# Optimization experiments

Measured on AMD Instinct MI355X. Metric: run time of the kernel, lower is better.

## Reference

```python
import jax, jax.numpy as jnp
import numpy as np

B, N = 4, 1024
D_MODEL, N_HEADS, D_HEAD, D_COORD = 512, 8, 64, 2


def setup_inputs() -> dict:
    key = jax.random.key(0)
    ks = jax.random.split(key, 8)
    sd = 1.0 / np.sqrt(D_MODEL)
    return {
        "x": jax.random.normal(ks[0], (B, N, D_MODEL), dtype=jnp.float32),
        "positions": jax.random.uniform(ks[1], (N, D_COORD), dtype=jnp.float32) * 32.0,
        "W_Q": jax.random.normal(ks[2], (D_MODEL, N_HEADS * D_HEAD), dtype=jnp.float32) * sd,
        "W_K": jax.random.normal(ks[3], (D_MODEL, N_HEADS * D_HEAD), dtype=jnp.float32) * sd,
        "W_V": jax.random.normal(ks[4], (D_MODEL, N_HEADS * D_HEAD), dtype=jnp.float32) * sd,
        "W_O": jax.random.normal(ks[5], (N_HEADS * D_HEAD, D_MODEL), dtype=jnp.float32) * sd,
        "U": jax.random.normal(ks[6], (N_HEADS, D_HEAD, D_HEAD), dtype=jnp.float32),
        "freqs": jax.random.normal(ks[7], (N_HEADS, D_HEAD // 2, D_COORD), dtype=jnp.float32),
    }


def reference(x, positions, W_Q, W_K, W_V, W_O, U, freqs):
    # x: (B,N,d_model); positions: (N,d_coord); U: (H,dh,dh); freqs: (H,m,d_coord)
    Bn, Nn, _ = x.shape
    H, dh, _ = U.shape
    m = dh // 2
    scale = (dh // 2) ** -0.5

    Q = (x @ W_Q).reshape(Bn, Nn, H, dh)
    K = (x @ W_K).reshape(Bn, Nn, H, dh)
    V = (x @ W_V).reshape(Bn, Nn, H, dh)

    # Active-subspace projector: Pi = qr(U)[0] @ qr(U)[0].T per head
    Uq = jax.vmap(lambda u: jnp.linalg.qr(u)[0])(U)              # (H,dh,dh)
    P = jnp.einsum('hde,hfe->hdf', Uq, Uq)                       # U U^T
    Qp = jnp.einsum('bnhd,hdf->bhnf', Q, P)                      # (B,H,N,dh)
    Kp = jnp.einsum('bnhd,hdf->bhnf', K, P)

    # Relative rotation: R_rel(r_j - r_i) is block-diag 2x2 rotations with
    # angle theta_ijm = freqs_m . (r_j - r_i) = a_jm - a_im (separable), so
    # q^T R(r_j-r_i) k = (R(a_i)q)^T (R(a_j)k)  -- exact RoPE identity.
    ang = jnp.einsum('nc,hmc->hnm', positions, freqs)            # (H,N,m)
    c = jnp.cos(ang)[None]                                       # (1,H,N,m)
    s = jnp.sin(ang)[None]

    def rot(v):  # v: (B,H,N,dh) -> rotated (even, odd) halves (B,H,N,m)
        ve, vo = v[..., ::2], v[..., 1::2]
        return ve * c - vo * s, ve * s + vo * c

    qe, qo = rot(Qp)
    ke, ko = rot(Kp)
    scores = (jnp.einsum('bhim,bhjm->bhij', qe, ke)
              + jnp.einsum('bhim,bhjm->bhij', qo, ko)) * scale   # (B,H,N,N)
    w = jax.nn.softmax(scores, axis=-1)
    out = jnp.einsum('bhij,bjhd->bihd', w, V).reshape(Bn, Nn, H * dh)
    return out @ W_O
```

## Files before the change

### kernel.cpp

```cpp
#include <hip/hip_runtime.h>
#include <hip/hip_bf16.h>
#include <math.h>

#define NBATCH 4
#define NSEQ   1024
#define DMODEL 512
#define NH     8
#define DH     64
#define MROWS  (NBATCH*NSEQ)
#define MHALF  (DH/2)

typedef __attribute__((ext_vector_type(8))) short bf16x8;
typedef __attribute__((ext_vector_type(4))) float floatx4;

__device__ __forceinline__ ushort f2bf(float f) {
    union { float f; uint u; } v; v.f = f;
    uint r = v.u + 0x7fffu + ((v.u >> 16) & 1u);
    return (ushort)(r >> 16);
}

__device__ __forceinline__ uint f2bf2(float lo, float hi) {
    union { __hip_bfloat162 h; uint u; } v;
    v.h = __float22bfloat162_rn(make_float2(lo, hi));
    return v.u;
}

__global__ __launch_bounds__(256) void prep_kernel(
    const float* __restrict__ pos, const float* __restrict__ freqs,
    const float* __restrict__ x,
    const float* __restrict__ Wq, const float* __restrict__ Wk,
    const float* __restrict__ Wv, const float* __restrict__ Wo,
    float* __restrict__ cosT, float* __restrict__ sinT,
    ushort* __restrict__ xb, ushort* __restrict__ Wt)
{
    __shared__ float T[64][65];
    const int bid = blockIdx.x;
    const int tid = threadIdx.x;

    if (bid < 1024) {
        int idx = bid * 256 + tid;
        int m = idx & 31;
        int n = (idx >> 5) & 1023;
        int h = idx >> 15;
        float a = pos[n*2+0] * freqs[(h*MHALF+m)*2+0]
                + pos[n*2+1] * freqs[(h*MHALF+m)*2+1];
        cosT[idx] = cosf(a);
        sinT[idx] = sinf(a);
    } else if (bid < 2048) {
        int idx = ((bid - 1024) * 256 + tid) * 8;
        float4 a = *(const float4*)&x[idx];
        float4 b = *(const float4*)&x[idx+4];
        uint4 pk;
        pk.x = f2bf2(a.x, a.y);
        pk.y = f2bf2(a.z, a.w);
        pk.z = f2bf2(b.x, b.y);
        pk.w = f2bf2(b.z, b.w);
        *(uint4*)&xb[idx] = pk;
    } else {
        int b2 = bid - 2048;
        int n0g = (b2 & 31) * 64;
        int k0  = (b2 >> 5) * 64;
        int mat = n0g >> 9;
        const float* W = (mat == 0) ? Wq : ((mat == 1) ? Wk : ((mat == 2) ? Wv : Wo));
        int n0 = n0g & 511;
        int c = tid & 63, r = tid >> 6;
        #pragma unroll
        for (int i = 0; i < 16; i++)
            T[r + i*4][c] = W[(k0 + r + i*4) * DMODEL + n0 + c];
        __syncthreads();
        int nl = tid >> 2;
        int kg = tid & 3;
        #pragma unroll
        for (int g = 0; g < 4; g++) {
            int kl = kg * 16 + g * 4;
            uint2 pk;
            pk.x = f2bf2(T[kl+0][nl], T[kl+1][nl]);
            pk.y = f2bf2(T[kl+2][nl], T[kl+3][nl]);
            *(uint2*)&Wt[(size_t)(n0g + nl) * DMODEL + k0 + kl] = pk;
        }
    }
}

__global__ __launch_bounds__(256) void qkv_gemm(
    const ushort* __restrict__ xb, const ushort* __restrict__ Wt,
    const float* __restrict__ cosT, const float* __restrict__ sinT,
    ushort* __restrict__ Qb, ushort* __restrict__ Kb, ushort* __restrict__ Vt)
{
    __shared__ ushort As[64 * 40];
    __shared__ ushort Bs[64 * 40];
    __shared__ float  Cs[64][65];

    const int cb = blockIdx.x;
    const int rb = blockIdx.y;
    const int mat = cb >> 3;
    const int c0 = (cb & 7) * 64;
    const int r0 = rb * 64;
    const int ng0 = mat * 512 + c0;

    const int tid = threadIdx.x;
    const int w = tid >> 6, l = tid & 63;
    const int lr = l & 15, lg = l >> 4;

    const int srow = tid >> 2;
    const int sgrp = tid & 3;

    floatx4 acc[4];
    #pragma unroll
    for (int nt = 0; nt < 4; nt++) acc[nt] = (floatx4){0.f,0.f,0.f,0.f};

    uint4 ra  = *(const uint4*)&xb[(size_t)(r0 + srow) * DMODEL + sgrp*8];
    uint4 rb2 = *(const uint4*)&Wt[(size_t)(ng0 + srow) * DMODEL + sgrp*8];

    for (int k0 = 0; k0 < DMODEL; k0 += 32) {
        __syncthreads();
        *(uint4*)&As[srow*40 + sgrp*8] = ra;
        *(uint4*)&Bs[srow*40 + sgrp*8] = rb2;
        __syncthreads();

        if (k0 + 32 < DMODEL) {
            ra  = *(const uint4*)&xb[(size_t)(r0 + srow) * DMODEL + k0 + 32 + sgrp*8];
            rb2 = *(const uint4*)&Wt[(size_t)(ng0 + srow) * DMODEL + k0 + 32 + sgrp*8];
        }

        bf16x8 af = *(const bf16x8*)&As[(16*w + lr)*40 + lg*8];
        #pragma unroll
        for (int nt = 0; nt < 4; nt++) {
            bf16x8 bf = *(const bf16x8*)&Bs[(nt*16 + lr)*40 + lg*8];
            acc[nt] = __builtin_amdgcn_mfma_f32_16x16x32_bf16(af, bf, acc[nt], 0, 0, 0);
        }
    }

    __syncthreads();
    #pragma unroll
    for (int nt = 0; nt < 4; nt++)
        #pragma unroll
        for (int r = 0; r < 4; r++)
            Cs[16*w + lg*4 + r][nt*16 + lr] = acc[nt][r];
    __syncthreads();

    const int tx = tid & 15, ty = tid >> 4;
    const int dbase = tx * 4;
    const int head = c0 >> 6;

    if (mat == 2) {
        int rowbase = r0 + ty * 4;
        int b = rowbase >> 10, n0 = rowbase & 1023;
        size_t vbase = (size_t)(b * NH + head) * DH;
        #pragma unroll
        for (int j = 0; j < 4; j++) {
            uint2 pk;
            pk.x = f2bf2(Cs[ty*4 + 0][tx*4 + j], Cs[ty*4 + 1][tx*4 + j]);
            pk.y = f2bf2(Cs[ty*4 + 2][tx*4 + j], Cs[ty*4 + 3][tx*4 + j]);
            *(uint2*)&Vt[(vbase + dbase + j) * NSEQ + n0] = pk;
        }
    } else {
        ushort* dst = (mat == 0) ? Qb : Kb;
        const float qs = (mat == 0) ? 0.17677669529663687f : 1.0f;
        #pragma unroll
        for (int i = 0; i < 4; i++) {
            int row = r0 + ty * 4 + i;
            int b = row >> 10, n = row & 1023;
            float v[4];
            #pragma unroll
            for (int p = 0; p < 2; p++) {
                int de = dbase + 2 * p;
                int m = de >> 1;
                float c = cosT[(head * NSEQ + n) * MHALF + m] * qs;
                float s = sinT[(head * NSEQ + n) * MHALF + m] * qs;
                float ve = Cs[ty*4 + i][tx*4 + 2*p];
                float vo = Cs[ty*4 + i][tx*4 + 2*p + 1];
                v[2*p]     = ve * c - vo * s;
                v[2*p + 1] = ve * s + vo * c;
            }
            uint2 pk;
            pk.x = f2bf2(v[0], v[1]);
            pk.y = f2bf2(v[2], v[3]);
            *(uint2*)&dst[((size_t)(b * NH + head) * NSEQ + n) * DH + dbase] = pk;
        }
    }
}

__global__ __launch_bounds__(256, 4) void attn_kernel(
    const ushort* __restrict__ Qb, const ushort* __restrict__ Kb,
    const ushort* __restrict__ Vt, float* __restrict__ Opart,
    float* __restrict__ Ml)
{
    __shared__ ushort Ks[64 * 72];
    __shared__ ushort Vs[64 * 72];
    __shared__ ushort Ps[64 * 72];

    const int tid = threadIdx.x;
    const int w = tid >> 6, l = tid & 63;
    const int lr = l & 15, lg = l >> 4;
    const int bh = blockIdx.y, q0 = blockIdx.x * 64;
    const int z = blockIdx.z, jt0 = z * 8;

    const ushort* Qg = Qb + (size_t)bh * NSEQ * DH;
    const ushort* Kg = Kb + (size_t)bh * NSEQ * DH;
    const ushort* Vg = Vt + (size_t)bh * DH * NSEQ;

    bf16x8 qf[2];
    #pragma unroll
    for (int ks = 0; ks < 2; ks++)
        qf[ks] = *(const bf16x8*)(Qg + (size_t)(q0 + 16*w + lr) * DH + ks*32 + lg*8);

    floatx4 ot[4];
    #pragma unroll
    for (int i = 0; i < 4; i++) ot[i] = (floatx4){0.f, 0.f, 0.f, 0.f};
    float l_lane = 0.f;

    const int sr = tid >> 2;
    const int sc = (tid & 3) * 16;

    const ushort* kp = Kg + (size_t)(jt0*64 + sr) * DH + sc;
    uint4 ka  = *(const uint4*)kp;
    uint4 kb2 = *(const uint4*)(kp + 8);
    const ushort* vp = Vg + (size_t)sr * NSEQ + jt0*64 + sc;
    uint4 va  = *(const uint4*)vp;
    uint4 vb2 = *(const uint4*)(vp + 8);

    for (int jt = jt0; jt < jt0 + 8; jt++) {
        __syncthreads();
        *(uint4*)&Ks[sr*72 + sc]     = ka;
        *(uint4*)&Ks[sr*72 + sc + 8] = kb2;
        *(uint4*)&Vs[sr*72 + sc]     = va;
        *(uint4*)&Vs[sr*72 + sc + 8] = vb2;
        __syncthreads();

        if (jt < jt0 + 7) {
            const ushort* kn = Kg + (size_t)((jt+1)*64 + sr) * DH + sc;
            ka  = *(const uint4*)kn;
            kb2 = *(const uint4*)(kn + 8);
            const ushort* vn = Vg + (size_t)sr * NSEQ + (jt+1)*64 + sc;
            va  = *(const uint4*)vn;
            vb2 = *(const uint4*)(vn + 8);
        }

        floatx4 st[4];
        #pragma unroll
        for (int jm = 0; jm < 4; jm++) {
            floatx4 acc = (floatx4){0.f, 0.f, 0.f, 0.f};
            #pragma unroll
            for (int ks = 0; ks < 2; ks++) {
                bf16x8 af = *(const bf16x8*)&Ks[(jm*16 + lr)*72 + ks*32 + lg*8];
                acc = __builtin_amdgcn_mfma_f32_16x16x32_bf16(af, qf[ks], acc, 0, 0, 0);
            }
            st[jm] = acc;
        }

        #pragma unroll
        for (int jm = 0; jm < 4; jm++) {
            float p0 = __expf(st[jm][0]);
            float p1 = __expf(st[jm][1]);
            float p2 = __expf(st[jm][2]);
            float p3 = __expf(st[jm][3]);
            l_lane += (p0 + p1) + (p2 + p3);
            uint2 pk;
            pk.x = f2bf2(p0, p1);
            pk.y = f2bf2(p2, p3);
            *(uint2*)&Ps[(16*w + lr)*72 + jm*16 + lg*4] = pk;
        }

        bf16x8 pf[2];
        #pragma unroll
        for (int ks = 0; ks < 2; ks++)
            pf[ks] = *(const bf16x8*)&Ps[(16*w + lr)*72 + ks*32 + lg*8];
        #pragma unroll
        for (int dt = 0; dt < 4; dt++)
            #pragma unroll
            for (int ks = 0; ks < 2; ks++) {
                bf16x8 af = *(const bf16x8*)&Vs[(dt*16 + lr)*72 + ks*32 + lg*8];
                ot[dt] = __builtin_amdgcn_mfma_f32_16x16x32_bf16(af, pf[ks], ot[dt], 0, 0, 0);
            }
    }

    l_lane += __shfl_xor(l_lane, 16, 64);
    l_lane += __shfl_xor(l_lane, 32, 64);

    int n = q0 + 16*w + lr;
    size_t obase = ((size_t)(z * 32 + bh) * NSEQ + n) * DH;
    #pragma unroll
    for (int dt = 0; dt < 4; dt++)
        *(floatx4*)&Opart[obase + dt*16 + lg*4] = ot[dt];
    if (lg == 0)
        Ml[(size_t)(z * 32 + bh) * NSEQ + n] = l_lane;
}

__global__ __launch_bounds__(256) void out_gemm(
    const float* __restrict__ Op, const float* __restrict__ Ml,
    const ushort* __restrict__ Wt, float* __restrict__ out)
{
    __shared__ ushort As[64 * 40];
    __shared__ ushort Bs[64 * 40];
    __shared__ float  Cs[64][65];

    const int cb = blockIdx.x;
    const int rb = blockIdx.y;
    const int c0 = cb * 64, r0 = rb * 64;

    const int tid = threadIdx.x;
    const int w = tid >> 6, l = tid & 63;
    const int lr = l & 15, lg = l >> 4;
    const int srow = tid >> 2;
    const int sgrp = tid & 3;

    const int arow = r0 + srow;
    const int b = arow >> 10, n = arow & 1023;

    floatx4 acc[4];
    #pragma unroll
    for (int nt = 0; nt < 4; nt++) acc[nt] = (floatx4){0.f,0.f,0.f,0.f};

    float4 u0, u1, v0, v1;
    float  lsum;
    uint4  rbv, pk;

    #define LOAD_A(K0) do {                                               \
        int h_  = (K0) >> 6;                                              \
        int dd_ = ((K0) & 63) + sgrp*8;                                   \
        size_t qi_ = (size_t)(b*NH + h_) * NSEQ + n;                      \
        const float* p1_ = Op + qi_*64 + dd_;                             \
        u0 = *(const float4*)p1_;                                         \
        u1 = *(const float4*)(p1_ + 4);                                   \
        v0 = *(const float4*)(p1_ + 2097152);                             \
        v1 = *(const float4*)(p1_ + 2097152 + 4);                         \
        lsum = Ml[qi_] + Ml[qi_ + 32768];                                 \
    } while (0)

    #define COMPUTE_PK() do {                                             \
        float inv = __builtin_amdgcn_rcpf(lsum);                          \
        pk.x = f2bf2((u0.x + v0.x) * inv, (u0.y + v0.y) * inv);           \
        pk.y = f2bf2((u0.z + v0.z) * inv, (u0.w + v0.w) * inv);           \
        pk.z = f2bf2((u1.x + v1.x) * inv, (u1.y + v1.y) * inv);           \
        pk.w = f2bf2((u1.z + v1.z) * inv, (u1.w + v1.w) * inv);           \
    } while (0)

    LOAD_A(0);
    rbv = *(const uint4*)&Wt[(size_t)(1536 + c0 + srow) * DMODEL + sgrp*8];
    COMPUTE_PK();

    for (int k0 = 0; k0 < DMODEL; k0 += 32) {
        __syncthreads();
        *(uint4*)&As[srow*40 + sgrp*8] = pk;
        *(uint4*)&Bs[srow*40 + sgrp*8] = rbv;
        __syncthreads();

        const bool more = (k0 + 32 < DMODEL);
        if (more) {
            LOAD_A(k0 + 32);
            rbv = *(const uint4*)&Wt[(size_t)(1536 + c0 + srow) * DMODEL + (k0 + 32) + sgrp*8];
        }

        bf16x8 af = *(const bf16x8*)&As[(16*w + lr)*40 + lg*8];
        #pragma unroll
        for (int nt = 0; nt < 4; nt++) {
            bf16x8 bf = *(const bf16x8*)&Bs[(nt*16 + lr)*40 + lg*8];
            acc[nt] = __builtin_amdgcn_mfma_f32_16x16x32_bf16(af, bf, acc[nt], 0, 0, 0);
        }

        if (more) COMPUTE_PK();
    }
    #undef LOAD_A
    #undef COMPUTE_PK

    __syncthreads();
    #pragma unroll
    for (int nt = 0; nt < 4; nt++)
        #pragma unroll
        for (int r = 0; r < 4; r++)
            Cs[16*w + lg*4 + r][nt*16 + lr] = acc[nt][r];
    __syncthreads();

    const int tx = tid & 15, ty = tid >> 4;
    #pragma unroll
    for (int i = 0; i < 4; i++) {
        float4 o;
        o.x = Cs[ty*4 + i][tx*4 + 0];
        o.y = Cs[ty*4 + i][tx*4 + 1];
        o.z = Cs[ty*4 + i][tx*4 + 2];
        o.w = Cs[ty*4 + i][tx*4 + 3];
        *(float4*)&out[(size_t)(r0 + ty*4 + i) * DMODEL + c0 + tx*4] = o;
    }
}

extern "C" void kernel_launch(void* const* d_in, const int* in_sizes, int n_in,
                              void* d_out, int out_size, void* d_ws, size_t ws_size,
                              hipStream_t stream) {
    const float* x         = (const float*)d_in[0];
    const float* positions = (const float*)d_in[1];
    const float* Wq        = (const float*)d_in[2];
    const float* Wk        = (const float*)d_in[3];
    const float* Wv        = (const float*)d_in[4];
    const float* Wo        = (const float*)d_in[5];
    const float* freqs     = (const float*)d_in[7];
    float* out = (float*)d_out;

    float*  ws    = (float*)d_ws;
    float*  cosT  = ws;
    float*  sinT  = cosT + NH*NSEQ*MHALF;
    float*  Opart = sinT + NH*NSEQ*MHALF;
    float*  Ml    = Opart + 2*(size_t)NBATCH*NH*NSEQ*DH;
    ushort* xb    = (ushort*)(Ml + 2*(size_t)NBATCH*NH*NSEQ);
    ushort* Wt    = xb + (size_t)MROWS*DMODEL;
    ushort* Qb    = Wt + (size_t)2048*DMODEL;
    ushort* Kb    = Qb + (size_t)NBATCH*NH*NSEQ*DH;
    ushort* Vt    = Kb + (size_t)NBATCH*NH*NSEQ*DH;

    prep_kernel<<<dim3(2304), 256, 0, stream>>>(positions, freqs, x, Wq, Wk, Wv, Wo,
                                                cosT, sinT, xb, Wt);
    qkv_gemm<<<dim3(24, 64), 256, 0, stream>>>(xb, Wt, cosT, sinT, Qb, Kb, Vt);
    attn_kernel<<<dim3(16, 32, 2), 256, 0, stream>>>(Qb, Kb, Vt, Opart, Ml);
    out_gemm<<<dim3(8, 64), 256, 0, stream>>>(Opart, Ml, Wt, out);
}
```

Before: 134.5 us.

## Drop split-K attention; normalize and store bf16 output directly

Attention no longer splits the key range into two halves. Each block now walks all 16 key tiles, normalizes by the row sum and writes a bf16 output. The out-projection GEMM then reads that bf16 tensor directly instead of combining two fp32 partials and row sums. This removes the fp32 partial write/read traffic and the combine work, but halves the attention grid to 512 blocks, which may underfill the 256 CUs and lengthen each block's serial loop.

Result: faster. 125.4 us (-6.7%).

```diff
diff --git a/kernel.cpp b/kernel.cpp
--- a/kernel.cpp
+++ b/kernel.cpp
@@ -12,12 +12,6 @@
 
 typedef __attribute__((ext_vector_type(8))) short bf16x8;
 typedef __attribute__((ext_vector_type(4))) float floatx4;
-
-__device__ __forceinline__ ushort f2bf(float f) {
-    union { float f; uint u; } v; v.f = f;
-    uint r = v.u + 0x7fffu + ((v.u >> 16) & 1u);
-    return (ushort)(r >> 16);
-}
 
 __device__ __forceinline__ uint f2bf2(float lo, float hi) {
     union { __hip_bfloat162 h; uint u; } v;
@@ -182,8 +176,7 @@
 
 __global__ __launch_bounds__(256, 4) void attn_kernel(
     const ushort* __restrict__ Qb, const ushort* __restrict__ Kb,
-    const ushort* __restrict__ Vt, float* __restrict__ Opart,
-    float* __restrict__ Ml)
+    const ushort* __restrict__ Vt, ushort* __restrict__ Obb)
 {
     __shared__ ushort Ks[64 * 72];
     __shared__ ushort Vs[64 * 72];
@@ -193,7 +186,6 @@
     const int w = tid >> 6, l = tid & 63;
     const int lr = l & 15, lg = l >> 4;
     const int bh = blockIdx.y, q0 = blockIdx.x * 64;
-    const int z = blockIdx.z, jt0 = z * 8;
 
     const ushort* Qg = Qb + (size_t)bh * NSEQ * DH;
     const ushort* Kg = Kb + (size_t)bh * NSEQ * DH;
@@ -212,14 +204,14 @@
     const int sr = tid >> 2;
     const int sc = (tid & 3) * 16;
 
-    const ushort* kp = Kg + (size_t)(jt0*64 + sr) * DH + sc;
+    const ushort* kp = Kg + (size_t)sr * DH + sc;
     uint4 ka  = *(const uint4*)kp;
     uint4 kb2 = *(const uint4*)(kp + 8);
-    const ushort* vp = Vg + (size_t)sr * NSEQ + jt0*64 + sc;
+    const ushort* vp = Vg + (size_t)sr * NSEQ + sc;
     uint4 va  = *(const uint4*)vp;
     uint4 vb2 = *(const uint4*)(vp + 8);
 
-    for (int jt = jt0; jt < jt0 + 8; jt++) {
+    for (int jt = 0; jt < 16; jt++) {
         __syncthreads();
         *(uint4*)&Ks[sr*72 + sc]     = ka;
         *(uint4*)&Ks[sr*72 + sc + 8] = kb2;
@@ -227,7 +219,7 @@
         *(uint4*)&Vs[sr*72 + sc + 8] = vb2;
         __syncthreads();
 
-        if (jt < jt0 + 7) {
+        if (jt < 15) {
             const ushort* kn = Kg + (size_t)((jt+1)*64 + sr) * DH + sc;
             ka  = *(const uint4*)kn;
             kb2 = *(const uint4*)(kn + 8);
@@ -276,19 +268,22 @@
 
     l_lane += __shfl_xor(l_lane, 16, 64);
     l_lane += __shfl_xor(l_lane, 32, 64);
+    float inv = 1.f / l_lane;
 
     int n = q0 + 16*w + lr;
-    size_t obase = ((size_t)(z * 32 + bh) * NSEQ + n) * DH;
-    #pragma unroll
-    for (int dt = 0; dt < 4; dt++)
-        *(floatx4*)&Opart[obase + dt*16 + lg*4] = ot[dt];
-    if (lg == 0)
-        Ml[(size_t)(z * 32 + bh) * NSEQ + n] = l_lane;
+    size_t obase = ((size_t)bh * NSEQ + n) * DH;
+    #pragma unroll
+    for (int dt = 0; dt < 4; dt++) {
+        uint2 pk;
+        pk.x = f2bf2(ot[dt][0] * inv, ot[dt][1] * inv);
+        pk.y = f2bf2(ot[dt][2] * inv, ot[dt][3] * inv);
+        *(uint2*)&Obb[obase + dt*16 + lg*4] = pk;
+    }
 }
 
 __global__ __launch_bounds__(256) void out_gemm(
-    const float* __restrict__ Op, const float* __restrict__ Ml,
-    const ushort* __restrict__ Wt, float* __restrict__ out)
+    const ushort* __restrict__ Obb, const ushort* __restrict__ Wt,
+    float* __restrict__ out)
 {
     __shared__ ushort As[64 * 40];
     __shared__ ushort Bs[64 * 40];
@@ -311,43 +306,19 @@
     #pragma unroll
     for (int nt = 0; nt < 4; nt++) acc[nt] = (floatx4){0.f,0.f,0.f,0.f};
 
-    float4 u0, u1, v0, v1;
-    float  lsum;
-    uint4  rbv, pk;
-
-    #define LOAD_A(K0) do {                                               \
-        int h_  = (K0) >> 6;                                              \
-        int dd_ = ((K0) & 63) + sgrp*8;                                   \
-        size_t qi_ = (size_t)(b*NH + h_) * NSEQ + n;                      \
-        const float* p1_ = Op + qi_*64 + dd_;                             \
-        u0 = *(const float4*)p1_;                                         \
-        u1 = *(const float4*)(p1_ + 4);                                   \
-        v0 = *(const float4*)(p1_ + 2097152);                             \
-        v1 = *(const float4*)(p1_ + 2097152 + 4);                         \
-        lsum = Ml[qi_] + Ml[qi_ + 32768];                                 \
-    } while (0)
-
-    #define COMPUTE_PK() do {                                             \
-        float inv = __builtin_amdgcn_rcpf(lsum);                          \
-        pk.x = f2bf2((u0.x + v0.x) * inv, (u0.y + v0.y) * inv);           \
-        pk.y = f2bf2((u0.z + v0.z) * inv, (u0.w + v0.w) * inv);           \
-        pk.z = f2bf2((u1.x + v1.x) * inv, (u1.y + v1.y) * inv);           \
-        pk.w = f2bf2((u1.z + v1.z) * inv, (u1.w + v1.w) * inv);           \
-    } while (0)
-
-    LOAD_A(0);
-    rbv = *(const uint4*)&Wt[(size_t)(1536 + c0 + srow) * DMODEL + sgrp*8];
-    COMPUTE_PK();
+    #define A_ADDR(K0) (&Obb[((size_t)(b*NH + ((K0) >> 6)) * NSEQ + n) * DH + ((K0) & 63) + sgrp*8])
+
+    uint4 rav = *(const uint4*)A_ADDR(0);
+    uint4 rbv = *(const uint4*)&Wt[(size_t)(1536 + c0 + srow) * DMODEL + sgrp*8];
 
     for (int k0 = 0; k0 < DMODEL; k0 += 32) {
         __syncthreads();
-        *(uint4*)&As[srow*40 + sgrp*8] = pk;
+        *(uint4*)&As[srow*40 + sgrp*8] = rav;
         *(uint4*)&Bs[srow*40 + sgrp*8] = rbv;
         __syncthreads();
 
-        const bool more = (k0 + 32 < DMODEL);
-        if (more) {
-            LOAD_A(k0 + 32);
+        if (k0 + 32 < DMODEL) {
+            rav = *(const uint4*)A_ADDR(k0 + 32);
             rbv = *(const uint4*)&Wt[(size_t)(1536 + c0 + srow) * DMODEL + (k0 + 32) + sgrp*8];
         }
 
@@ -357,11 +328,8 @@
             bf16x8 bf = *(const bf16x8*)&Bs[(nt*16 + lr)*40 + lg*8];
             acc[nt] = __builtin_amdgcn_mfma_f32_16x16x32_bf16(af, bf, acc[nt], 0, 0, 0);
         }
-
-        if (more) COMPUTE_PK();
-    }
-    #undef LOAD_A
-    #undef COMPUTE_PK
+    }
+    #undef A_ADDR
 
     __syncthreads();
     #pragma unroll
@@ -398,17 +366,16 @@
     float*  ws    = (float*)d_ws;
     float*  cosT  = ws;
     float*  sinT  = cosT + NH*NSEQ*MHALF;
-    float*  Opart = sinT + NH*NSEQ*MHALF;
-    float*  Ml    = Opart + 2*(size_t)NBATCH*NH*NSEQ*DH;
-    ushort* xb    = (ushort*)(Ml + 2*(size_t)NBATCH*NH*NSEQ);
+    ushort* xb    = (ushort*)(sinT + NH*NSEQ*MHALF);
     ushort* Wt    = xb + (size_t)MROWS*DMODEL;
     ushort* Qb    = Wt + (size_t)2048*DMODEL;
     ushort* Kb    = Qb + (size_t)NBATCH*NH*NSEQ*DH;
     ushort* Vt    = Kb + (size_t)NBATCH*NH*NSEQ*DH;
+    ushort* Obb   = Vt + (size_t)NBATCH*NH*NSEQ*DH;
 
     prep_kernel<<<dim3(2304), 256, 0, stream>>>(positions, freqs, x, Wq, Wk, Wv, Wo,
                                                 cosT, sinT, xb, Wt);
     qkv_gemm<<<dim3(24, 64), 256, 0, stream>>>(xb, Wt, cosT, sinT, Qb, Kb, Vt);
-    attn_kernel<<<dim3(16, 32, 2), 256, 0, stream>>>(Qb, Kb, Vt, Opart, Ml);
-    out_gemm<<<dim3(8, 64), 256, 0, stream>>>(Opart, Ml, Wt, out);
-}
+    attn_kernel<<<dim3(16, 32), 256, 0, stream>>>(Qb, Kb, Vt, Obb);
+    out_gemm<<<dim3(8, 64), 256, 0, stream>>>(Obb, Wt, out);
+}
```
